# Kernel optimization log

Hardware: AMD Instinct MI355X
Metric: run time of the kernel (lower is better)

## Reference

```python
import jax, jax.numpy as jnp
import numpy as np
from math import sqrt

B, LD, LS, CS, CH, H, PQ, PV = 4, 512, 512, 384, 16, 12, 4, 8
EPS, INF = 1e-8, 1e5
W_C = sqrt(2.0 / (9.0 * PQ))
W_L = sqrt(0.5)
SOFTPLUS_INV_1 = 0.5413248546129181  # ipa_point_weights_init_: softplus(hw)=1


def _rand_rot(k, shape):
    m = jax.random.normal(k, shape + (3, 3), dtype=jnp.float32)
    q, r = jnp.linalg.qr(m)
    # fix sign so det is well conditioned (any orthogonal matrix is fine for a rigid frame)
    d = jnp.sign(jnp.diagonal(r, axis1=-2, axis2=-1))
    return q * d[..., None, :]


def setup_inputs() -> dict:
    key = jax.random.key(0)
    ks = jax.random.split(key, 16)
    s_dst = jax.random.normal(ks[0], (B, LD, CS), dtype=jnp.float32)
    s_src = jax.random.normal(ks[1], (B, LS, CS), dtype=jnp.float32)
    R_dst = _rand_rot(ks[2], (B, LD))
    t_dst = jax.random.normal(ks[3], (B, LD, 3), dtype=jnp.float32)
    R_src = _rand_rot(ks[4], (B, LS))
    t_src = jax.random.normal(ks[5], (B, LS, 3), dtype=jnp.float32)
    dst_mask = jnp.ones((B, LD), dtype=bool)
    src_mask = jnp.ones((B, LS), dtype=bool)
    sc = 1.0 / sqrt(CS)
    Wq = jax.random.normal(ks[6], (CS, H * CH), dtype=jnp.float32) * sc
    Wkv = jax.random.normal(ks[7], (CS, 2 * H * CH), dtype=jnp.float32) * sc
    Wqp = jax.random.normal(ks[8], (CS, H * PQ * 3), dtype=jnp.float32) * sc
    Wkvp = jax.random.normal(ks[9], (CS, H * (PQ + PV) * 3), dtype=jnp.float32) * sc
    cat_dim = H * (CH + PV * 4)
    Wout = jax.random.normal(ks[10], (cat_dim, CS), dtype=jnp.float32) * (1.0 / sqrt(cat_dim))
    b_out = jnp.zeros((CS,), dtype=jnp.float32)
    head_weights = jnp.full((H,), SOFTPLUS_INV_1, dtype=jnp.float32)
    return dict(s_dst=s_dst, s_src=s_src, R_dst=R_dst, t_dst=t_dst, R_src=R_src,
                t_src=t_src, dst_mask=dst_mask, src_mask=src_mask, Wq=Wq, Wkv=Wkv,
                Wqp=Wqp, Wkvp=Wkvp, Wout=Wout, b_out=b_out, head_weights=head_weights)


def _points(s, W, R, t, n_pts):
    # linear -> 3 chunks of H*n_pts stacked on last axis, then rigid apply
    b, l = s.shape[0], s.shape[1]
    p = (s @ W).reshape(b, l, 3, H * n_pts)          # chunk axis first
    p = jnp.swapaxes(p, -1, -2)                      # [B, L, H*n_pts, 3]
    p = jnp.einsum('blij,blpj->blpi', R, p) + t[:, :, None, :]
    return p.reshape(b, l, H, n_pts, 3)


def reference(s_dst, s_src, R_dst, t_dst, R_src, t_src, dst_mask, src_mask,
              Wq, Wkv, Wqp, Wkvp, Wout, b_out, head_weights):
    q = (s_dst @ Wq).reshape(B, LD, H, CH)
    kv = (s_src @ Wkv).reshape(B, LS, H, 2 * CH)
    k, v = kv[..., :CH], kv[..., CH:]

    q_pts = _points(s_dst, Wqp, R_dst, t_dst, PQ)                 # [B,LD,H,PQ,3]
    kv_pts = _points(s_src, Wkvp, R_src, t_src, PQ + PV)          # [B,LS,H,PQ+PV,3]
    k_pts, v_pts = kv_pts[..., :PQ, :], kv_pts[..., PQ:, :]

    a_sd = jnp.einsum('bihc,bjhc->bhij', q, k) * (1.0 / sqrt(CH))

    # sum_{p,d} (q-k)^2 = |q|^2 + |k|^2 - 2 q.k  (avoids [B,LD,LS,H,PQ,3] blowup)
    q2 = jnp.sum(q_pts ** 2, axis=(-1, -2))                       # [B,LD,H]
    k2 = jnp.sum(k_pts ** 2, axis=(-1, -2))                       # [B,LS,H]
    qk = jnp.einsum('bihpd,bjhpd->bhij', q_pts, k_pts)
    d2 = jnp.transpose(q2, (0, 2, 1))[..., None] + jnp.transpose(k2, (0, 2, 1))[:, :, None, :] - 2.0 * qk

    hw = jax.nn.softplus(head_weights)                            # [H]
    a_pt = 0.5 * W_C * hw[None, :, None, None] * d2               # [B,H,LD,LS]

    sq_mask = dst_mask[:, :, None] & src_mask[:, None, :]         # [B,LD,LS]
    bias = INF * (~sq_mask).astype(s_dst.dtype)
    a = jax.nn.softmax(W_L * (a_sd - a_pt) - bias[:, None, :, :], axis=-1)

    o = jnp.einsum('bhij,bjhc->bihc', a, v).reshape(B, LD, H * CH)
    o_pt = jnp.einsum('bhij,bjhpd->bihpd', a, v_pts)              # [B,LD,H,PV,3]
    # invert_apply: R^T (x - t)
    o_pt = jnp.einsum('blji,blhpj->blhpi', R_dst, o_pt - t_dst[:, :, None, None, :])
    o_pt_norm = jnp.sqrt(jnp.sum(o_pt ** 2, axis=-1) + EPS).reshape(B, LD, H * PV)
    o_pt = o_pt.reshape(B, LD, H * PV, 3)

    cat = jnp.concatenate([o, o_pt[..., 0], o_pt[..., 1], o_pt[..., 2], o_pt_norm], axis=-1)
    s_upd = cat @ Wout + b_out
    return s_upd, a
```

## Files before the change

### kernel.cpp

```cpp
#include <hip/hip_runtime.h>
#include <math.h>

#define B_   4
#define LD_  512
#define LS_  512
#define CS_  384
#define CH_  16
#define H_   12
#define PQ_  4
#define PV_  8
#define EPS_ 1e-8f
#define W_C_ 0.23570226039551584f
#define W_L_ 0.7071067811865476f

typedef __attribute__((ext_vector_type(8))) short short8_t;
typedef __attribute__((ext_vector_type(4))) float f32x4;

__device__ __forceinline__ ushort f2bf(float f) {
  unsigned u = __builtin_bit_cast(unsigned, f);
  unsigned r = (u + 0x7FFFu + ((u >> 16) & 1u)) >> 16;
  return (ushort)r;
}
__device__ __forceinline__ float bf2f_us(ushort us) {
  return __builtin_bit_cast(float, (unsigned)us << 16);
}
__device__ __forceinline__ float bf2f_lo(unsigned u) {
  return __builtin_bit_cast(float, u << 16);
}
__device__ __forceinline__ float bf2f_hi(unsigned u) {
  return __builtin_bit_cast(float, u & 0xffff0000u);
}

__global__ __launch_bounds__(256) void mgemm_proj_k(
    const float* __restrict__ s_dst, const float* __restrict__ s_src,
    const float* __restrict__ Wq, const float* __restrict__ Wqp,
    const float* __restrict__ Wkv, const float* __restrict__ Wkvp,
    ushort* __restrict__ qextg, float* __restrict__ rawp_d,
    ushort* __restrict__ kextg, ushort* __restrict__ vextg,
    float* __restrict__ rawp_s) {
  __shared__ ushort Asub[4][64][8];
  __shared__ ushort Bsub[4][128][8];
  int bid = blockIdx.x;
  const float* A; int Ntot, mode, nt, mt;
  const float *W1, *W2; int N1, ld1, ld2;
  if (bid < 96) {
    nt = bid % 3; mt = bid / 3; A = s_dst; Ntot = 336; mode = 0;
    W1 = Wq; W2 = Wqp; N1 = 192; ld1 = 192; ld2 = 144;
  } else {
    bid -= 96; nt = bid % 7; mt = bid / 7; A = s_src; Ntot = 816; mode = 1;
    W1 = Wkv; W2 = Wkvp; N1 = 384; ld1 = 384; ld2 = 432;
  }
  const int K = 384;
  const int m0 = mt * 64, n0 = nt * 128;
  const int t = threadIdx.x;
  const int w = t >> 6, g = (t >> 4) & 3, li = t & 15;
  const int sarow = t & 63, sakc = t >> 6;
  const float* arow = A + (size_t)(m0 + sarow) * K + sakc * 8;
  const int sbrow = t & 127, sbkc = t >> 7;
  const int ncl = (n0 + sbrow < Ntot) ? (n0 + sbrow) : (Ntot - 1);
  const float* Wb; int ldw;
  if (ncl < N1) { Wb = W1 + ncl; ldw = ld1; } else { Wb = W2 + (ncl - N1); ldw = ld2; }
  const float* wptr0 = Wb + (size_t)(sbkc * 8) * ldw;
  const float* wptr1 = Wb + (size_t)((sbkc + 2) * 8) * ldw;
  const int wm = (w & 1) * 32, wn = (w >> 1) * 64;

  f32x4 acc[2][4];
  #pragma unroll
  for (int ms = 0; ms < 2; ++ms)
    #pragma unroll
    for (int ns = 0; ns < 4; ++ns) { acc[ms][ns][0]=0.f; acc[ms][ns][1]=0.f; acc[ms][ns][2]=0.f; acc[ms][ns][3]=0.f; }

  float4 af0 = *(const float4*)(arow);
  float4 af1 = *(const float4*)(arow + 4);
  float wv0[8], wv1[8];
  #pragma unroll
  for (int j = 0; j < 8; ++j) { wv0[j] = wptr0[(size_t)j * ldw]; wv1[j] = wptr1[(size_t)j * ldw]; }

  for (int k0 = 0; k0 < K; k0 += 32) {
    union { short8_t v; ushort u[8]; } av, bv0, bv1;
    av.u[0]=f2bf(af0.x); av.u[1]=f2bf(af0.y); av.u[2]=f2bf(af0.z); av.u[3]=f2bf(af0.w);
    av.u[4]=f2bf(af1.x); av.u[5]=f2bf(af1.y); av.u[6]=f2bf(af1.z); av.u[7]=f2bf(af1.w);
    #pragma unroll
    for (int j = 0; j < 8; ++j) { bv0.u[j] = f2bf(wv0[j]); bv1.u[j] = f2bf(wv1[j]); }
    __syncthreads();
    *(short8_t*)&Asub[sakc][sarow][0] = av.v;
    *(short8_t*)&Bsub[sbkc][sbrow][0] = bv0.v;
    *(short8_t*)&Bsub[sbkc + 2][sbrow][0] = bv1.v;
    if (k0 + 32 < K) {
      af0 = *(const float4*)(arow + k0 + 32);
      af1 = *(const float4*)(arow + k0 + 36);
      const float* wp0 = wptr0 + (size_t)(k0 + 32) * ldw;
      const float* wp1 = wptr1 + (size_t)(k0 + 32) * ldw;
      #pragma unroll
      for (int j = 0; j < 8; ++j) { wv0[j] = wp0[(size_t)j * ldw]; wv1[j] = wp1[(size_t)j * ldw]; }
    }
    __syncthreads();
    #pragma unroll
    for (int ms = 0; ms < 2; ++ms) {
      const short8_t afr = *(const short8_t*)&Asub[g][wm + ms * 16 + li][0];
      #pragma unroll
      for (int ns = 0; ns < 4; ++ns) {
        const short8_t bfr = *(const short8_t*)&Bsub[g][wn + ns * 16 + li][0];
        acc[ms][ns] = __builtin_amdgcn_mfma_f32_16x16x32_bf16(afr, bfr, acc[ms][ns], 0, 0, 0);
      }
    }
  }

  const float qsc = 0.25f * W_L_;
  #pragma unroll
  for (int ms = 0; ms < 2; ++ms) {
    #pragma unroll
    for (int ns = 0; ns < 4; ++ns) {
      const int gn = n0 + wn + ns * 16 + li;
      if (gn >= Ntot) continue;
      #pragma unroll
      for (int r = 0; r < 4; ++r) {
        const int gm = m0 + wm + ms * 16 + g * 4 + r;
        const int bb = gm >> 9, rr = gm & 511;
        const float v = acc[ms][ns][r];
        if (mode == 0) {
          if (gn < 192) {
            const int h = gn >> 4, cc = gn & 15;
            qextg[(((size_t)(bb * H_ + h) * 4 + (cc >> 3)) * 512 + rr) * 8 + (cc & 7)] = f2bf(qsc * v);
          } else rawp_d[(size_t)gm * 144 + gn - 192] = v;
        } else {
          if (gn < 384) {
            const int h = gn >> 5, cc = gn & 31;
            if (cc < 16)
              kextg[(((size_t)(bb * H_ + h) * 4 + (cc >> 3)) * 512 + rr) * 8 + (cc & 7)] = f2bf(v);
            else
              vextg[((size_t)(bb * H_ + h) * 48 + (cc - 16)) * 512 + rr] = f2bf(v);
          } else rawp_s[(size_t)gm * 432 + gn - 384] = v;
        }
      }
    }
  }
}

__global__ __launch_bounds__(256) void pack_k(
    const float* __restrict__ rawp_d, const float* __restrict__ rawp_s,
    const float* __restrict__ R_dst, const float* __restrict__ t_dst,
    const float* __restrict__ R_src, const float* __restrict__ t_src,
    const float* __restrict__ head_weights, const float* __restrict__ Wout,
    ushort* __restrict__ qextg, ushort* __restrict__ kextg,
    ushort* __restrict__ vextg, ushort* __restrict__ Wt_out) {
  __shared__ float sq[8][48];
  int bid = blockIdx.x;
  const int t = threadIdx.x;
  if (bid >= 384) {
    const int cid = bid - 384;
    const int nt = cid % 6, kt = cid / 6;
    const int n = nt * 64 + (t & 63);
    const int k0 = kt * 32 + (t >> 6) * 8;
    union { short8_t v; ushort u[8]; } o;
    #pragma unroll
    for (int j = 0; j < 8; ++j) o.u[j] = f2bf(Wout[(size_t)(k0 + j) * 384 + n]);
    *(short8_t*)(Wt_out + (size_t)n * 576 + k0) = o.v;
    return;
  }
  if (bid < 128) {
    const int r0 = bid * 16;
    const int r = t >> 4, lp = t & 15;
    const int row = r0 + r;
    const float* Rm = R_dst + row * 9;
    const float* tv = t_dst + row * 3;
    const int b = row >> 9, irow = row & 511;
    #pragma unroll
    for (int pp = 0; pp < 3; ++pp) {
      const int p = lp + pp * 16;
      const float x = rawp_d[(size_t)row * 144 + p];
      const float y = rawp_d[(size_t)row * 144 + 48 + p];
      const float z = rawp_d[(size_t)row * 144 + 96 + p];
      float o[3];
      o[0] = Rm[0] * x + Rm[1] * y + Rm[2] * z + tv[0];
      o[1] = Rm[3] * x + Rm[4] * y + Rm[5] * z + tv[1];
      o[2] = Rm[6] * x + Rm[7] * y + Rm[8] * z + tv[2];
      const int h = p >> 2, pt = p & 3;
      const float hw = head_weights[h];
      const float coef = 0.5f * W_C_ * logf(1.f + __expf(hw));
      const float qpsc = 2.f * W_L_ * coef;
      const size_t bh4 = (size_t)(b * H_ + h) * 4;
      #pragma unroll
      for (int d = 0; d < 3; ++d) {
        const int cidx = pt * 3 + d;
        const int plane = (cidx >= 8) ? 3 : 2;
        const int elem = (cidx >= 8) ? cidx - 8 : cidx;
        qextg[((bh4 + plane) * 512 + irow) * 8 + elem] = f2bf(qpsc * o[d]);
      }
      if (pt == 0) {
        unsigned* up = (unsigned*)(qextg + ((bh4 + 3) * 512 + irow) * 8);
        up[2] = 0x3F803F80u;
        up[3] = 0u;
      }
    }
  } else {
    bid -= 128;
    const int r0 = bid * 8;
    const int r = t >> 5, l = t & 31;
    const int row = r0 + r;
    const float* Rm = R_src + row * 9;
    const float* tv = t_src + row * 3;
    const int b = row >> 9, jrow = row & 511;
    #pragma unroll
    for (int pp = 0; pp < 5; ++pp) {
      const int p = l + pp * 32;
      if (p < 144) {
        const float x = rawp_s[(size_t)row * 432 + p];
        const float y = rawp_s[(size_t)row * 432 + 144 + p];
        const float z = rawp_s[(size_t)row * 432 + 288 + p];
        float o[3];
        o[0] = Rm[0] * x + Rm[1] * y + Rm[2] * z + tv[0];
        o[1] = Rm[3] * x + Rm[4] * y + Rm[5] * z + tv[1];
        o[2] = Rm[6] * x + Rm[7] * y + Rm[8] * z + tv[2];
        const int h = p / 12, pt = p - h * 12;
        const size_t bh = (size_t)(b * H_ + h);
        if (pt < PQ_) {
          #pragma unroll
          for (int d = 0; d < 3; ++d) {
            const int cidx = pt * 3 + d;
            const int plane = (cidx >= 8) ? 3 : 2;
            const int elem = (cidx >= 8) ? cidx - 8 : cidx;
            kextg[((bh * 4 + plane) * 512 + jrow) * 8 + elem] = f2bf(o[d]);
          }
          sq[r][h * 4 + pt] = o[0] * o[0] + o[1] * o[1] + o[2] * o[2];
        } else {
          #pragma unroll
          for (int d = 0; d < 3; ++d)
            vextg[(bh * 48 + 16 + (pt - PQ_) * 3 + d) * 512 + jrow] = f2bf(o[d]);
        }
      }
    }
    __syncthreads();
    if (t < 96) {
      const int rr = t / 12, h = t % 12;
      const int grow = r0 + rr;
      const float k2 = sq[rr][h * 4] + sq[rr][h * 4 + 1] + sq[rr][h * 4 + 2] + sq[rr][h * 4 + 3];
      const float hw = head_weights[h];
      const float coef = 0.5f * W_C_ * logf(1.f + __expf(hw));
      const float c1 = -W_L_ * coef * k2;
      const ushort c1h = f2bf(c1);
      const ushort c1l = f2bf(c1 - bf2f_us(c1h));
      unsigned* up = (unsigned*)(kextg +
          (((size_t)((grow >> 9) * H_ + h) * 4 + 3) * 512 + (grow & 511)) * 8);
      up[2] = (unsigned)c1h | ((unsigned)c1l << 16);
      up[3] = 0u;
    }
  }
}

__global__ __launch_bounds__(256, 6) void attn_k(
    const ushort* __restrict__ qextg, const ushort* __restrict__ kextg,
    const ushort* __restrict__ vextg, const float* __restrict__ R_dst,
    const float* __restrict__ t_dst, float* __restrict__ a_out,
    ushort* __restrict__ catb) {
  __shared__ __align__(16) char smem[20736];
  ushort* alds  = (ushort*)smem;
  unsigned* alds32 = (unsigned*)smem;
  float* red    = (float*)(smem + 17408);
  float* fin    = (float*)(smem + 17664);

  const int sbid = (blockIdx.x & 7) * 192 + (blockIdx.x >> 3);
  const int it = sbid & 31;
  const int bh = sbid >> 5;
  const int h = bh % H_;
  const int b = bh / H_;
  const int i0 = it * 16;
  const int t = threadIdx.x;
  const int l = t & 63, w = t >> 6, g = l >> 4, li = l & 15;

  const short8_t bq = *(const short8_t*)(qextg + (((size_t)bh * 4 + g) * 512 + i0 + li) * 8);

  const ushort* kbase = kextg + ((size_t)bh * 4 + g) * 4096 + (size_t)(w * 128 + li) * 8;
  f32x4 sc[8];
  #pragma unroll
  for (int jt = 0; jt < 8; ++jt) {
    const short8_t af = *(const short8_t*)(kbase + jt * 128);
    f32x4 z; z[0]=0.f; z[1]=0.f; z[2]=0.f; z[3]=0.f;
    sc[jt] = __builtin_amdgcn_mfma_f32_16x16x32_bf16(af, bq, z, 0, 0, 0);
  }

  float mx = -1e30f;
  #pragma unroll
  for (int jt = 0; jt < 8; ++jt) {
    mx = fmaxf(mx, fmaxf(fmaxf(sc[jt][0], sc[jt][1]), fmaxf(sc[jt][2], sc[jt][3])));
  }
  mx = fmaxf(mx, __shfl_xor(mx, 16));
  mx = fmaxf(mx, __shfl_xor(mx, 32));
  if (g == 0) red[w * 16 + li] = mx;
  __syncthreads();
  mx = fmaxf(fmaxf(red[li], red[16 + li]), fmaxf(red[32 + li], red[48 + li]));
  float sm = 0.f;
  #pragma unroll
  for (int jt = 0; jt < 8; ++jt) {
    #pragma unroll
    for (int r = 0; r < 4; ++r) {
      const float e = __expf(sc[jt][r] - mx);
      sc[jt][r] = e;
      sm += e;
    }
  }
  sm += __shfl_xor(sm, 16);
  sm += __shfl_xor(sm, 32);
  __syncthreads();
  if (g == 0) red[w * 16 + li] = sm;
  __syncthreads();
  const float inv = 1.f / (red[li] + red[16 + li] + red[32 + li] + red[48 + li]);

  #pragma unroll
  for (int jt = 0; jt < 8; ++jt) {
    const float a0 = sc[jt][0] * inv, a1 = sc[jt][1] * inv;
    const float a2 = sc[jt][2] * inv, a3 = sc[jt][3] * inv;
    const unsigned p0 = (unsigned)f2bf(a0) | ((unsigned)f2bf(a1) << 16);
    const unsigned p1 = (unsigned)f2bf(a2) | ((unsigned)f2bf(a3) << 16);
    const int jpb = jt * 8 + g * 2;
    alds32[w * 1088 + li * 68 + jpb]     = p0;
    alds32[w * 1088 + li * 68 + jpb + 1] = p1;
  }
  __syncthreads();

  if (w == 3) {
    float* abase = a_out + ((size_t)bh * LD_ + i0) * LS_;
    #pragma unroll
    for (int u = 0; u < 32; ++u) {
      const int idx4 = (t - 192) + u * 64;
      const int i = idx4 >> 7, j4 = idx4 & 127;
      const int reg = j4 >> 5;
      const int jp = ((j4 * 4) & 127) >> 1;
      const unsigned u0 = alds32[reg * 1088 + i * 68 + jp];
      const unsigned u1 = alds32[reg * 1088 + i * 68 + jp + 1];
      float4 vv = make_float4(bf2f_lo(u0), bf2f_hi(u0), bf2f_lo(u1), bf2f_hi(u1));
      *(float4*)(abase + (size_t)i * 512 + j4 * 4) = vv;
    }
  } else {
    const int ct = w;
    f32x4 acc; acc[0]=0.f; acc[1]=0.f; acc[2]=0.f; acc[3]=0.f;
    const ushort* vbase = vextg + ((size_t)bh * 48 + ct * 16 + li) * 512 + g * 8;
    #pragma unroll
    for (int ch = 0; ch < 4; ++ch) {
      #pragma unroll
      for (int sub = 0; sub < 4; ++sub) {
        const short8_t afv = *(const short8_t*)(vbase + ch * 128 + sub * 32);
        const short8_t abf = *(const short8_t*)&alds[ch * 2176 + li * 136 + sub * 32 + g * 8];
        acc = __builtin_amdgcn_mfma_f32_16x16x32_bf16(afv, abf, acc, 0, 0, 0);
      }
    }
    #pragma unroll
    for (int r = 0; r < 4; ++r)
      fin[(ct * 16 + g * 4 + r) * 16 + li] = acc[r];
  }
  __syncthreads();

  const int drow0 = b * LD_ + i0;
  {
    const int i = t >> 4, c = t & 15;
    catb[(size_t)(drow0 + i) * 576 + h * 16 + c] = f2bf(fin[c * 16 + i]);
  }
  if (t < 128) {
    const int i = t >> 3, p = t & 7;
    const int drow = drow0 + i;
    const float* R = R_dst + drow * 9;
    const float* tv = t_dst + drow * 3;
    const float gx = fin[(16 + p * 3) * 16 + i]     - tv[0];
    const float gy = fin[(16 + p * 3 + 1) * 16 + i] - tv[1];
    const float gz = fin[(16 + p * 3 + 2) * 16 + i] - tv[2];
    const float lx = R[0] * gx + R[3] * gy + R[6] * gz;
    const float ly = R[1] * gx + R[4] * gy + R[7] * gz;
    const float lz = R[2] * gx + R[5] * gy + R[8] * gz;
    const float nrm = sqrtf(lx * lx + ly * ly + lz * lz + EPS_);
    ushort* catrow = catb + (size_t)drow * 576;
    const int hp = h * PV_ + p;
    catrow[192 + hp] = f2bf(lx);
    catrow[288 + hp] = f2bf(ly);
    catrow[384 + hp] = f2bf(lz);
    catrow[480 + hp] = f2bf(nrm);
  }
}

__global__ __launch_bounds__(256) void mgemm_out_k(
    const ushort* __restrict__ catb, const ushort* __restrict__ Wt_out,
    const float* __restrict__ bias, float* __restrict__ s_upd) {
  __shared__ ushort Asub[8][32][8];
  __shared__ ushort Bsub[8][64][8];
  const int nt = blockIdx.x % 6, mt = blockIdx.x / 6;
  const int K = 576;
  const int m0 = mt * 32, n0 = nt * 64;
  const int t = threadIdx.x;
  const int w = t >> 6, g = (t >> 4) & 3, li = t & 15;
  const int sarow = t & 31, sakc = t >> 5;
  const int sbrow = t & 63, sbkc = t >> 6;
  const ushort* arow = catb + (size_t)(m0 + sarow) * K + sakc * 8;
  const ushort* wrow0 = Wt_out + (size_t)(n0 + sbrow) * K + sbkc * 8;
  const ushort* wrow1 = wrow0 + 32;
  const int wm = (w & 1) * 16, wn = (w >> 1) * 32;

  f32x4 acc[2];
  #pragma unroll
  for (int ns = 0; ns < 2; ++ns) { acc[ns][0]=0.f; acc[ns][1]=0.f; acc[ns][2]=0.f; acc[ns][3]=0.f; }

  short8_t av = *(const short8_t*)(arow);
  short8_t bv0 = *(const short8_t*)(wrow0);
  short8_t bv1 = *(const short8_t*)(wrow1);

  for (int k0 = 0; k0 < K; k0 += 64) {
    const short8_t acur = av, bcur0 = bv0, bcur1 = bv1;
    __syncthreads();
    *(short8_t*)&Asub[sakc][sarow][0] = acur;
    *(short8_t*)&Bsub[sbkc][sbrow][0] = bcur0;
    *(short8_t*)&Bsub[sbkc + 4][sbrow][0] = bcur1;
    if (k0 + 64 < K) {
      av  = *(const short8_t*)(arow + k0 + 64);
      bv0 = *(const short8_t*)(wrow0 + k0 + 64);
      bv1 = *(const short8_t*)(wrow1 + k0 + 64);
    }
    __syncthreads();
    #pragma unroll
    for (int s = 0; s < 2; ++s) {
      const short8_t afr = *(const short8_t*)&Asub[s * 4 + g][wm + li][0];
      #pragma unroll
      for (int ns = 0; ns < 2; ++ns) {
        const short8_t bfr = *(const short8_t*)&Bsub[s * 4 + g][wn + ns * 16 + li][0];
        acc[ns] = __builtin_amdgcn_mfma_f32_16x16x32_bf16(afr, bfr, acc[ns], 0, 0, 0);
      }
    }
  }

  #pragma unroll
  for (int ns = 0; ns < 2; ++ns) {
    const int gn = n0 + wn + ns * 16 + li;
    const float bo = bias[gn];
    #pragma unroll
    for (int r = 0; r < 4; ++r) {
      const int gm = m0 + wm + g * 4 + r;
      s_upd[(size_t)gm * 384 + gn] = acc[ns][r] + bo;
    }
  }
}

extern "C" void kernel_launch(void* const* d_in, const int* in_sizes, int n_in,
                              void* d_out, int out_size, void* d_ws, size_t ws_size,
                              hipStream_t stream) {
  const float* s_dst = (const float*)d_in[0];
  const float* s_src = (const float*)d_in[1];
  const float* R_dst = (const float*)d_in[2];
  const float* t_dst = (const float*)d_in[3];
  const float* R_src = (const float*)d_in[4];
  const float* t_src = (const float*)d_in[5];
  const float* Wq   = (const float*)d_in[8];
  const float* Wkv  = (const float*)d_in[9];
  const float* Wqp  = (const float*)d_in[10];
  const float* Wkvp = (const float*)d_in[11];
  const float* Wout = (const float*)d_in[12];
  const float* b_out = (const float*)d_in[13];
  const float* head_weights = (const float*)d_in[14];

  float* out = (float*)d_out;
  float* s_upd = out;
  float* a_out = out + (size_t)B_ * LD_ * CS_;

  float* ws = (float*)d_ws;
  float* rawp_d = ws;
  float* rawp_s = rawp_d + 294912;
  ushort* catb  = (ushort*)rawp_d;
  ushort* qextg = (ushort*)(rawp_s + 884736);
  ushort* kextg = qextg + 786432;
  ushort* vextg = kextg + 786432;
  ushort* Wt_out = vextg + 1179648;

  mgemm_proj_k<<<320, 256, 0, stream>>>(s_dst, s_src, Wq, Wqp, Wkv, Wkvp,
                                        qextg, rawp_d, kextg, vextg, rawp_s);
  pack_k<<<492, 256, 0, stream>>>(rawp_d, rawp_s, R_dst, t_dst, R_src, t_src,
                                  head_weights, Wout, qextg, kextg, vextg, Wt_out);
  attn_k<<<B_ * H_ * 32, 256, 0, stream>>>(qextg, kextg, vextg, R_dst, t_dst,
                                           a_out, catb);
  mgemm_out_k<<<384, 256, 0, stream>>>(catb, Wt_out, b_out, s_upd);
}
```

Before: 54.28 us.

## Fuse point rigid transform and packing into projection GEMM epilogue

Removes the separate pack kernel by reordering the weight columns so each point's x,y,z land in adjacent lanes. The projection GEMM epilogue then applies the rotation and translation with lane shuffles and writes the packed bf16 q/k/v point planes and the k2 bias directly. The Wout transpose-to-bf16 blocks move into the projection launch. This cuts one kernel launch and the fp32 raw-point round trip through global memory, at the cost of a heavier epilogue that does per-element R/t loads and shuffles, plus some padded columns in the source GEMM tiles.

```diff
diff --git a/kernel.cpp b/kernel.cpp
--- a/kernel.cpp
+++ b/kernel.cpp
@@ -33,33 +33,56 @@
 
 __global__ __launch_bounds__(256) void mgemm_proj_k(
     const float* __restrict__ s_dst, const float* __restrict__ s_src,
+    const float* __restrict__ R_dst, const float* __restrict__ t_dst,
+    const float* __restrict__ R_src, const float* __restrict__ t_src,
     const float* __restrict__ Wq, const float* __restrict__ Wqp,
     const float* __restrict__ Wkv, const float* __restrict__ Wkvp,
-    ushort* __restrict__ qextg, float* __restrict__ rawp_d,
-    ushort* __restrict__ kextg, ushort* __restrict__ vextg,
-    float* __restrict__ rawp_s) {
+    const float* __restrict__ Wout, const float* __restrict__ head_weights,
+    ushort* __restrict__ qextg, ushort* __restrict__ kextg,
+    ushort* __restrict__ vextg, ushort* __restrict__ Wt_out) {
+  const int t = threadIdx.x;
+  int bid = blockIdx.x;
+  if (bid >= 352) {
+    const int cid = bid - 352;
+    const int nt = cid % 6, kt = cid / 6;
+    const int n = nt * 64 + (t & 63);
+    const int k0 = kt * 32 + (t >> 6) * 8;
+    union { short8_t v; ushort u[8]; } o;
+    #pragma unroll
+    for (int j = 0; j < 8; ++j) o.u[j] = f2bf(Wout[(size_t)(k0 + j) * 384 + n]);
+    *(short8_t*)(Wt_out + (size_t)n * 576 + k0) = o.v;
+    return;
+  }
+
   __shared__ ushort Asub[4][64][8];
   __shared__ ushort Bsub[4][128][8];
-  int bid = blockIdx.x;
-  const float* A; int Ntot, mode, nt, mt;
-  const float *W1, *W2; int N1, ld1, ld2;
-  if (bid < 96) {
-    nt = bid % 3; mt = bid / 3; A = s_dst; Ntot = 336; mode = 0;
-    W1 = Wq; W2 = Wqp; N1 = 192; ld1 = 192; ld2 = 144;
-  } else {
-    bid -= 96; nt = bid % 7; mt = bid / 7; A = s_src; Ntot = 816; mode = 1;
-    W1 = Wkv; W2 = Wkvp; N1 = 384; ld1 = 384; ld2 = 432;
-  }
+  const float* A; int mode, nt, mt, pbase;
+  if (bid < 96) { nt = bid % 3; mt = bid / 3; A = s_dst; mode = 0; pbase = 192; }
+  else { bid -= 96; nt = bid % 8; mt = bid / 8; A = s_src; mode = 1; pbase = 384; }
   const int K = 384;
   const int m0 = mt * 64, n0 = nt * 128;
-  const int t = threadIdx.x;
-  const int w = t >> 6, g = (t >> 4) & 3, li = t & 15;
+  const int w = t >> 6, g = (t >> 4) & 3, li = t & 15, l = t & 63;
   const int sarow = t & 63, sakc = t >> 6;
   const float* arow = A + (size_t)(m0 + sarow) * K + sakc * 8;
   const int sbrow = t & 127, sbkc = t >> 7;
-  const int ncl = (n0 + sbrow < Ntot) ? (n0 + sbrow) : (Ntot - 1);
   const float* Wb; int ldw;
-  if (ncl < N1) { Wb = W1 + ncl; ldw = ld1; } else { Wb = W2 + (ncl - N1); ldw = ld2; }
+  {
+    const int c = n0 + sbrow;
+    if (mode == 0) {
+      if (c < 192) { Wb = Wq + c; ldw = 192; }
+      else {
+        const int pc = c - 192, pp = pc >> 2, d = pc & 3;
+        Wb = Wqp + ((d < 3) ? d * 48 + pp : pp); ldw = 144;
+      }
+    } else {
+      if (c < 384) { Wb = Wkv + c; ldw = 384; }
+      else {
+        int pc = c - 384; if (pc > 575) pc = 575;
+        const int pp = pc >> 2, d = pc & 3;
+        Wb = Wkvp + ((d < 3) ? d * 144 + pp : pp); ldw = 432;
+      }
+    }
+  }
   const float* wptr0 = Wb + (size_t)(sbkc * 8) * ldw;
   const float* wptr1 = Wb + (size_t)((sbkc + 2) * 8) * ldw;
   const int wm = (w & 1) * 32, wn = (w >> 1) * 64;
@@ -106,144 +129,107 @@
     }
   }
 
-  const float qsc = 0.25f * W_L_;
-  #pragma unroll
-  for (int ms = 0; ms < 2; ++ms) {
-    #pragma unroll
-    for (int ns = 0; ns < 4; ++ns) {
-      const int gn = n0 + wn + ns * 16 + li;
-      if (gn >= Ntot) continue;
-      #pragma unroll
-      for (int r = 0; r < 4; ++r) {
-        const int gm = m0 + wm + ms * 16 + g * 4 + r;
-        const int bb = gm >> 9, rr = gm & 511;
-        const float v = acc[ms][ns][r];
-        if (mode == 0) {
-          if (gn < 192) {
+  if (n0 + wn < pbase) {
+    const float qsc = 0.25f * W_L_;
+    #pragma unroll
+    for (int ms = 0; ms < 2; ++ms) {
+      #pragma unroll
+      for (int ns = 0; ns < 4; ++ns) {
+        const int gn = n0 + wn + ns * 16 + li;
+        #pragma unroll
+        for (int r = 0; r < 4; ++r) {
+          const int gm = m0 + wm + ms * 16 + g * 4 + r;
+          const int bb = gm >> 9, rr = gm & 511;
+          const float v = acc[ms][ns][r];
+          if (mode == 0) {
             const int h = gn >> 4, cc = gn & 15;
             qextg[(((size_t)(bb * H_ + h) * 4 + (cc >> 3)) * 512 + rr) * 8 + (cc & 7)] = f2bf(qsc * v);
-          } else rawp_d[(size_t)gm * 144 + gn - 192] = v;
-        } else {
-          if (gn < 384) {
+          } else {
             const int h = gn >> 5, cc = gn & 31;
             if (cc < 16)
               kextg[(((size_t)(bb * H_ + h) * 4 + (cc >> 3)) * 512 + rr) * 8 + (cc & 7)] = f2bf(v);
             else
               vextg[((size_t)(bb * H_ + h) * 48 + (cc - 16)) * 512 + rr] = f2bf(v);
-          } else rawp_s[(size_t)gm * 432 + gn - 384] = v;
+          }
         }
       }
     }
-  }
-}
-
-__global__ __launch_bounds__(256) void pack_k(
-    const float* __restrict__ rawp_d, const float* __restrict__ rawp_s,
-    const float* __restrict__ R_dst, const float* __restrict__ t_dst,
-    const float* __restrict__ R_src, const float* __restrict__ t_src,
-    const float* __restrict__ head_weights, const float* __restrict__ Wout,
-    ushort* __restrict__ qextg, ushort* __restrict__ kextg,
-    ushort* __restrict__ vextg, ushort* __restrict__ Wt_out) {
-  __shared__ float sq[8][48];
-  int bid = blockIdx.x;
-  const int t = threadIdx.x;
-  if (bid >= 384) {
-    const int cid = bid - 384;
-    const int nt = cid % 6, kt = cid / 6;
-    const int n = nt * 64 + (t & 63);
-    const int k0 = kt * 32 + (t >> 6) * 8;
-    union { short8_t v; ushort u[8]; } o;
-    #pragma unroll
-    for (int j = 0; j < 8; ++j) o.u[j] = f2bf(Wout[(size_t)(k0 + j) * 384 + n]);
-    *(short8_t*)(Wt_out + (size_t)n * 576 + k0) = o.v;
-    return;
-  }
-  if (bid < 128) {
-    const int r0 = bid * 16;
-    const int r = t >> 4, lp = t & 15;
-    const int row = r0 + r;
-    const float* Rm = R_dst + row * 9;
-    const float* tv = t_dst + row * 3;
-    const int b = row >> 9, irow = row & 511;
-    #pragma unroll
-    for (int pp = 0; pp < 3; ++pp) {
-      const int p = lp + pp * 16;
-      const float x = rawp_d[(size_t)row * 144 + p];
-      const float y = rawp_d[(size_t)row * 144 + 48 + p];
-      const float z = rawp_d[(size_t)row * 144 + 96 + p];
-      float o[3];
-      o[0] = Rm[0] * x + Rm[1] * y + Rm[2] * z + tv[0];
-      o[1] = Rm[3] * x + Rm[4] * y + Rm[5] * z + tv[1];
-      o[2] = Rm[6] * x + Rm[7] * y + Rm[8] * z + tv[2];
-      const int h = p >> 2, pt = p & 3;
-      const float hw = head_weights[h];
-      const float coef = 0.5f * W_C_ * logf(1.f + __expf(hw));
-      const float qpsc = 2.f * W_L_ * coef;
-      const size_t bh4 = (size_t)(b * H_ + h) * 4;
-      #pragma unroll
-      for (int d = 0; d < 3; ++d) {
-        const int cidx = pt * 3 + d;
-        const int plane = (cidx >= 8) ? 3 : 2;
-        const int elem = (cidx >= 8) ? cidx - 8 : cidx;
-        qextg[((bh4 + plane) * 512 + irow) * 8 + elem] = f2bf(qpsc * o[d]);
-      }
-      if (pt == 0) {
-        unsigned* up = (unsigned*)(qextg + ((bh4 + 3) * 512 + irow) * 8);
-        up[2] = 0x3F803F80u;
-        up[3] = 0u;
-      }
-    }
   } else {
-    bid -= 128;
-    const int r0 = bid * 8;
-    const int r = t >> 5, l = t & 31;
-    const int row = r0 + r;
-    const float* Rm = R_src + row * 9;
-    const float* tv = t_src + row * 3;
-    const int b = row >> 9, jrow = row & 511;
-    #pragma unroll
-    for (int pp = 0; pp < 5; ++pp) {
-      const int p = l + pp * 32;
-      if (p < 144) {
-        const float x = rawp_s[(size_t)row * 432 + p];
-        const float y = rawp_s[(size_t)row * 432 + 144 + p];
-        const float z = rawp_s[(size_t)row * 432 + 288 + p];
-        float o[3];
-        o[0] = Rm[0] * x + Rm[1] * y + Rm[2] * z + tv[0];
-        o[1] = Rm[3] * x + Rm[4] * y + Rm[5] * z + tv[1];
-        o[2] = Rm[6] * x + Rm[7] * y + Rm[8] * z + tv[2];
-        const int h = p / 12, pt = p - h * 12;
-        const size_t bh = (size_t)(b * H_ + h);
-        if (pt < PQ_) {
-          #pragma unroll
-          for (int d = 0; d < 3; ++d) {
-            const int cidx = pt * 3 + d;
-            const int plane = (cidx >= 8) ? 3 : 2;
-            const int elem = (cidx >= 8) ? cidx - 8 : cidx;
-            kextg[((bh * 4 + plane) * 512 + jrow) * 8 + elem] = f2bf(o[d]);
+    const float* Rbase = (mode == 0) ? R_dst : R_src;
+    const float* tbase = (mode == 0) ? t_dst : t_src;
+    const int e = li & 3;
+    const int ee = (e < 3) ? e : 0;
+    #pragma unroll
+    for (int ms = 0; ms < 2; ++ms) {
+      #pragma unroll
+      for (int ns = 0; ns < 4; ++ns) {
+        const int fc = n0 + wn + ns * 16;
+        const int p = (fc - pbase + (li & ~3)) >> 2;
+        if (mode == 1 && p >= 144) continue;
+        #pragma unroll
+        for (int r = 0; r < 4; ++r) {
+          const int gm = m0 + wm + ms * 16 + g * 4 + r;
+          const float v = acc[ms][ns][r];
+          const float x = __shfl(v, (l & ~3) | 0);
+          const float y = __shfl(v, (l & ~3) | 1);
+          const float z = __shfl(v, (l & ~3) | 2);
+          const float* Rm = Rbase + gm * 9;
+          const float* tv = tbase + gm * 3;
+          const float o = Rm[ee * 3] * x + Rm[ee * 3 + 1] * y + Rm[ee * 3 + 2] * z + tv[ee];
+          const float o0 = __shfl(o, (l & ~3) | 0);
+          const float o1 = __shfl(o, (l & ~3) | 1);
+          const float o2 = __shfl(o, (l & ~3) | 2);
+          const int bb = gm >> 9, rr = gm & 511;
+          if (mode == 0) {
+            const int h = p >> 2, pt = p & 3;
+            const size_t bh4 = (size_t)(bb * H_ + h) * 4;
+            if (e < 3) {
+              const float hw = head_weights[h];
+              const float coef = 0.5f * W_C_ * logf(1.f + __expf(hw));
+              const float qpsc = 2.f * W_L_ * coef;
+              const int cidx = pt * 3 + e;
+              const int plane = (cidx >= 8) ? 3 : 2;
+              const int elem = (cidx >= 8) ? cidx - 8 : cidx;
+              qextg[((bh4 + plane) * 512 + rr) * 8 + elem] = f2bf(qpsc * o);
+            } else if (pt == 0) {
+              unsigned* up = (unsigned*)(qextg + ((bh4 + 3) * 512 + rr) * 8);
+              up[2] = 0x3F803F80u;
+              up[3] = 0u;
+            }
+          } else {
+            const int h = p / 12, pt = p % 12;
+            const size_t bh = (size_t)(bb * H_ + h);
+            if (pt < PQ_) {
+              if (e < 3) {
+                const int cidx = pt * 3 + e;
+                const int plane = (cidx >= 8) ? 3 : 2;
+                const int elem = (cidx >= 8) ? cidx - 8 : cidx;
+                kextg[((bh * 4 + plane) * 512 + rr) * 8 + elem] = f2bf(o);
+              } else {
+                const float nsq = o0 * o0 + o1 * o1 + o2 * o2;
+                const float n0v = __shfl(nsq, (l & ~15) | 3);
+                const float n1v = __shfl(nsq, (l & ~15) | 7);
+                const float n2v = __shfl(nsq, (l & ~15) | 11);
+                const float n3v = __shfl(nsq, (l & ~15) | 15);
+                if (li == 15) {
+                  const float k2 = ((n0v + n1v) + n2v) + n3v;
+                  const float hw = head_weights[h];
+                  const float coef = 0.5f * W_C_ * logf(1.f + __expf(hw));
+                  const float c1 = -W_L_ * coef * k2;
+                  const ushort c1h = f2bf(c1);
+                  const ushort c1l = f2bf(c1 - bf2f_us(c1h));
+                  unsigned* up = (unsigned*)(kextg + ((bh * 4 + 3) * 512 + rr) * 8);
+                  up[2] = (unsigned)c1h | ((unsigned)c1l << 16);
+                  up[3] = 0u;
+                }
+              }
+            } else {
+              if (e < 3)
+                vextg[(bh * 48 + 16 + (pt - PQ_) * 3 + e) * 512 + rr] = f2bf(o);
+            }
           }
-          sq[r][h * 4 + pt] = o[0] * o[0] + o[1] * o[1] + o[2] * o[2];
-        } else {
-          #pragma unroll
-          for (int d = 0; d < 3; ++d)
-            vextg[(bh * 48 + 16 + (pt - PQ_) * 3 + d) * 512 + jrow] = f2bf(o[d]);
         }
       }
-    }
-    __syncthreads();
-    if (t < 96) {
-      const int rr = t / 12, h = t % 12;
-      const int grow = r0 + rr;
-      const float k2 = sq[rr][h * 4] + sq[rr][h * 4 + 1] + sq[rr][h * 4 + 2] + sq[rr][h * 4 + 3];
-      const float hw = head_weights[h];
-      const float coef = 0.5f * W_C_ * logf(1.f + __expf(hw));
-      const float c1 = -W_L_ * coef * k2;
-      const ushort c1h = f2bf(c1);
-      const ushort c1l = f2bf(c1 - bf2f_us(c1h));
-      unsigned* up = (unsigned*)(kextg +
-          (((size_t)((grow >> 9) * H_ + h) * 4 + 3) * 512 + (grow & 511)) * 8);
-      up[2] = (unsigned)c1h | ((unsigned)c1l << 16);
-      up[3] = 0u;
     }
   }
 }
@@ -457,19 +443,15 @@
   float* s_upd = out;
   float* a_out = out + (size_t)B_ * LD_ * CS_;
 
-  float* ws = (float*)d_ws;
-  float* rawp_d = ws;
-  float* rawp_s = rawp_d + 294912;
-  ushort* catb  = (ushort*)rawp_d;
-  ushort* qextg = (ushort*)(rawp_s + 884736);
+  ushort* catb  = (ushort*)d_ws;
+  ushort* qextg = catb + 1179648;
   ushort* kextg = qextg + 786432;
   ushort* vextg = kextg + 786432;
   ushort* Wt_out = vextg + 1179648;
 
-  mgemm_proj_k<<<320, 256, 0, stream>>>(s_dst, s_src, Wq, Wqp, Wkv, Wkvp,
-                                        qextg, rawp_d, kextg, vextg, rawp_s);
-  pack_k<<<492, 256, 0, stream>>>(rawp_d, rawp_s, R_dst, t_dst, R_src, t_src,
-                                  head_weights, Wout, qextg, kextg, vextg, Wt_out);
+  mgemm_proj_k<<<460, 256, 0, stream>>>(s_dst, s_src, R_dst, t_dst, R_src, t_src,
+                                        Wq, Wqp, Wkv, Wkvp, Wout, head_weights,
+                                        qextg, kextg, vextg, Wt_out);
   attn_k<<<B_ * H_ * 32, 256, 0, stream>>>(qextg, kextg, vextg, R_dst, t_dst,
                                            a_out, catb);
   mgemm_out_k<<<384, 256, 0, stream>>>(catb, Wt_out, b_out, s_upd);
```

Measured after the change: 66.54 us. +22.6%, slower.
